# Performance work log

Measured on AMD Instinct MI355X. Metric: run time of the kernel, lower is better.

The kernel has to match this reference:

```python
import jax, jax.numpy as jnp
import numpy as np

B, NS, NT, C = 32, 1000, 100, 256
LAMBDA_GIOU, LAMBDA_L1 = 10.0, 1.0


def _lsa(cost):
    """Hungarian / Jonker-Volgenant shortest-augmenting-path (numpy, O(n^2 m)).
    Matches scipy.optimize.linear_sum_assignment for rectangular matrices."""
    cost = np.asarray(cost, dtype=np.float64)
    transposed = cost.shape[0] > cost.shape[1]
    if transposed:
        cost = cost.T
    n, m = cost.shape  # n <= m
    INF = np.inf
    u = np.zeros(n + 1)
    v = np.zeros(m + 1)
    p = np.zeros(m + 1, dtype=np.int64)   # p[j] = row (1-based) assigned to col j
    way = np.zeros(m + 1, dtype=np.int64)
    for i in range(1, n + 1):
        p[0] = i
        j0 = 0
        minv = np.full(m + 1, INF)
        used = np.zeros(m + 1, dtype=bool)
        while True:
            used[j0] = True
            i0 = p[j0]
            cur = cost[i0 - 1, :] - u[i0] - v[1:]
            free = ~used[1:]
            better = free & (cur < minv[1:])
            minv[1:][better] = cur[better]
            way[1:][better] = j0
            masked = np.where(free, minv[1:], INF)
            j1 = int(np.argmin(masked)) + 1
            delta = masked[j1 - 1]
            u[p[used]] += delta
            v[used] -= delta
            minv[~used] -= delta
            j0 = j1
            if p[j0] == 0:
                break
        while j0:
            j1 = way[j0]
            p[j0] = p[j1]
            j0 = j1
    rows = p[1:] - 1
    cols = np.arange(m)
    keep = rows >= 0
    rows, cols = rows[keep], cols[keep]
    if transposed:
        rows, cols = cols, rows
    order = np.argsort(rows)
    return rows[order], cols[order]


def _pairwise_cost(logits, classes, sb, tb):
    """Per-batch (Ns,Nt) cost = CE(logits_s, class_t) + 10*(1-GIoU(box_s, box_t)) + L1mean."""
    Bc, Ns, Cd = logits.shape
    Nt = classes.shape[1]
    # Cross entropy: logsumexp over classes minus logit at target class (identical
    # math to the torch expand+flatten CE, without the Ns*Nt*C copy).
    lse = jax.nn.logsumexp(logits, axis=-1)  # (B,Ns)
    picked = jnp.take_along_axis(
        logits, jnp.broadcast_to(classes[:, None, :], (Bc, Ns, Nt)), axis=2)  # (B,Ns,Nt)
    ce = lse[:, :, None] - picked
    # Pairwise GIoU (boxes in xyxy)
    s = sb[:, :, None, :]  # (B,Ns,1,4)
    t = tb[:, None, :, :]  # (B,1,Nt,4)
    ix1 = jnp.maximum(s[..., 0], t[..., 0])
    iy1 = jnp.maximum(s[..., 1], t[..., 1])
    ix2 = jnp.minimum(s[..., 2], t[..., 2])
    iy2 = jnp.minimum(s[..., 3], t[..., 3])
    inter = jnp.clip(ix2 - ix1, 0.0) * jnp.clip(iy2 - iy1, 0.0)
    area_s = (s[..., 2] - s[..., 0]) * (s[..., 3] - s[..., 1])
    area_t = (t[..., 2] - t[..., 0]) * (t[..., 3] - t[..., 1])
    union = area_s + area_t - inter
    iou = inter / union
    cx1 = jnp.minimum(s[..., 0], t[..., 0])
    cy1 = jnp.minimum(s[..., 1], t[..., 1])
    cx2 = jnp.maximum(s[..., 2], t[..., 2])
    cy2 = jnp.maximum(s[..., 3], t[..., 3])
    carea = (cx2 - cx1) * (cy2 - cy1)
    giou = iou - (carea - union) / carea
    l1 = jnp.abs(s - t).mean(axis=-1)  # (B,Ns,Nt)
    return ce + LAMBDA_GIOU * (1.0 - giou) + LAMBDA_L1 * l1


def _valid_boxes(key, b, n):
    p = jax.random.uniform(key, (b, n, 2, 2), dtype=jnp.float32)
    lo = p.min(axis=2)
    hi = p.max(axis=2)
    return jnp.concatenate([lo, hi], axis=-1)  # (b,n,4) xyxy, x1<x2, y1<y2


def setup_inputs() -> dict:
    key = jax.random.key(0)
    k1, k2, k3, k4 = jax.random.split(key, 4)
    return {
        "source_class_logits": jax.random.normal(k1, (B, NS, C), dtype=jnp.float32),
        "target_classes": jax.random.randint(k2, (B, NT), 0, C, dtype=jnp.int32),
        "source_boxes": _valid_boxes(k3, B, NS),
        "target_boxes": _valid_boxes(k4, B, NT),
    }


def reference(source_class_logits, target_classes, source_boxes, target_boxes):
    cost = _pairwise_cost(source_class_logits, target_classes, source_boxes, target_boxes)
    cost_np = np.asarray(cost)
    rows_l, cols_l = [], []
    for b in range(cost_np.shape[0]):  # assignment is inherently per-matrix / host-side
        r, c = _lsa(cost_np[b])
        rows_l.append(r)
        cols_l.append(c)
    rows = jnp.asarray(np.stack(rows_l))  # (B, min(Ns,Nt))
    cols = jnp.asarray(np.stack(cols_l))
    bidx = jnp.arange(cost.shape[0])[:, None]
    return cost[bidx, rows, cols].mean(axis=1)  # (B,)
```

## Files before the change

### kernel.cpp

```cpp
#include <hip/hip_runtime.h>
#include <math.h>

#define NSRC 1000
#define NTGT 100
#define NCLS 256
#define NB   32
#define NSP  1024
#define PAD_IDX(j) ((j) + ((j) >> 4))
#define LDSN (NSP + (NSP >> 4))
#define AUCTION_EPS 0.01f

__global__ __launch_bounds__(256) void lse_kernel(const float* __restrict__ logits,
                                                  float* __restrict__ lse) {
    int wid  = threadIdx.x >> 6;
    int lane = threadIdx.x & 63;
    int row0 = blockIdx.x * 32 + wid * 8;
    #pragma unroll 2
    for (int r = 0; r < 8; ++r) {
        int row = row0 + r;
        float4 v4 = reinterpret_cast<const float4*>(logits + (size_t)row * NCLS)[lane];
        float m = fmaxf(fmaxf(v4.x, v4.y), fmaxf(v4.z, v4.w));
        #pragma unroll
        for (int off = 32; off >= 1; off >>= 1) m = fmaxf(m, __shfl_xor(m, off));
        float s = expf(v4.x - m) + expf(v4.y - m) + expf(v4.z - m) + expf(v4.w - m);
        #pragma unroll
        for (int off = 32; off >= 1; off >>= 1) s += __shfl_xor(s, off);
        if (lane == 0) lse[row] = m + logf(s);
    }
}

__global__ __launch_bounds__(256) void cost_kernel(const float* __restrict__ logits,
                                                   const int*   __restrict__ tcls,
                                                   const float* __restrict__ sbox,
                                                   const float* __restrict__ tbox,
                                                   const float* __restrict__ lse,
                                                   float*       __restrict__ cost,
                                                   float*       __restrict__ urow_g,
                                                   int*         __restrict__ jmin_g,
                                                   float*       __restrict__ m2_g) {
    int b  = blockIdx.x & 31;
    int t  = blockIdx.x >> 5;
    int bt = b * NTGT + t;
    int cls = tcls[bt];
    float4 tb = reinterpret_cast<const float4*>(tbox)[bt];
    float area_t = (tb.z - tb.x) * (tb.w - tb.y);
    float* crow = cost + (size_t)bt * NSP;
    float m1 = 1e38f, m2 = 1e38f; int mi = 0x7fffffff;
    for (int s = threadIdx.x; s < NSP; s += 256) {
        if (s >= NSRC) { crow[s] = 1e30f; continue; }
        int gs = b * NSRC + s;
        float4 sb = reinterpret_cast<const float4*>(sbox)[gs];
        float ce = lse[gs] - logits[(size_t)gs * NCLS + cls];
        float ix1 = fmaxf(sb.x, tb.x), iy1 = fmaxf(sb.y, tb.y);
        float ix2 = fminf(sb.z, tb.z), iy2 = fminf(sb.w, tb.w);
        float inter = fmaxf(ix2 - ix1, 0.f) * fmaxf(iy2 - iy1, 0.f);
        float area_s = (sb.z - sb.x) * (sb.w - sb.y);
        float uni = area_s + area_t - inter;
        float iou = inter / uni;
        float cx1 = fminf(sb.x, tb.x), cy1 = fminf(sb.y, tb.y);
        float cx2 = fmaxf(sb.z, tb.z), cy2 = fmaxf(sb.w, tb.w);
        float carea = (cx2 - cx1) * (cy2 - cy1);
        float giou = iou - (carea - uni) / carea;
        float l1 = 0.25f * (fabsf(sb.x - tb.x) + fabsf(sb.y - tb.y) +
                            fabsf(sb.z - tb.z) + fabsf(sb.w - tb.w));
        float c = ce + 10.0f * (1.0f - giou) + l1;
        crow[s] = c;
        if (c < m1) { m2 = m1; m1 = c; mi = s; }
        else if (c < m2) m2 = c;
    }
    #pragma unroll
    for (int off = 32; off >= 1; off >>= 1) {
        float om1 = __shfl_xor(m1, off);
        float om2 = __shfl_xor(m2, off);
        int   oi  = __shfl_xor(mi, off);
        bool take = (om1 < m1) || (om1 == m1 && oi < mi);
        float lose = take ? m1 : om1;
        m1 = take ? om1 : m1;
        mi = take ? oi  : mi;
        m2 = fminf(fminf(m2, om2), lose);
    }
    __shared__ float smin[4], smin2[4];
    __shared__ int   sidx[4];
    int wid = threadIdx.x >> 6, lane = threadIdx.x & 63;
    if (lane == 0) { smin[wid] = m1; smin2[wid] = m2; sidx[wid] = mi; }
    __syncthreads();
    if (threadIdx.x == 0) {
        #pragma unroll
        for (int w = 1; w < 4; ++w) {
            float om1 = smin[w], om2 = smin2[w]; int oi = sidx[w];
            bool take = (om1 < m1) || (om1 == m1 && oi < mi);
            float lose = take ? m1 : om1;
            m1 = take ? om1 : m1;
            mi = take ? oi  : mi;
            m2 = fminf(fminf(m2, om2), lose);
        }
        urow_g[bt] = m1;
        jmin_g[bt] = mi;
        m2_g[bt]   = m2;
    }
}

__global__ __launch_bounds__(64) void lsa_kernel(const float* __restrict__ cost,
                                                 const float* __restrict__ urow_g,
                                                 const int*   __restrict__ jmin_g,
                                                 const float* __restrict__ m2_g,
                                                 float* __restrict__ out) {
    int b    = blockIdx.x;
    int lane = threadIdx.x;
    const float* C = cost + (size_t)b * NTGT * NSP;
    __shared__ int   way[LDSN];
    __shared__ int   pcol[LDSN];
    __shared__ float uu[LDSN];
    __shared__ float vsh[LDSN];
    __shared__ float urow[NTGT];
    __shared__ float m2s[NTGT];
    __shared__ int   jmin[NTGT];
    __shared__ int   done[NTGT];
    __shared__ int   queue[768];
    for (int t = lane; t < LDSN; t += 64) {
        pcol[t] = -1; uu[t] = 0.f; vsh[t] = 0.f; way[t] = 0x7fffffff;
    }
    for (int t = lane; t < NTGT; t += 64) {
        urow[t] = urow_g[b * NTGT + t];
        jmin[t] = jmin_g[b * NTGT + t];
        m2s[t]  = m2_g[b * NTGT + t];
    }
    float v[16], d[16];
    #pragma unroll
    for (int k = 0; k < 16; ++k) v[k] = 0.f;
    int base = lane * 16;
    __syncthreads();

    for (int r = lane; r < NTGT; r += 64) atomicMin(&way[PAD_IDX(jmin[r])], r);
    __syncthreads();
    for (int r = lane; r < NTGT; r += 64) {
        int j = jmin[r];
        int w = (way[PAD_IDX(j)] == r) ? 1 : 0;
        done[r] = w;
        if (w) { pcol[PAD_IDX(j)] = r; uu[PAD_IDX(j)] = urow[r]; }
    }
    __syncthreads();

    int qt = 0;
    #pragma unroll
    for (int r0 = 0; r0 < 128; r0 += 64) {
        int r = r0 + lane;
        bool act = (r < NTGT) && !done[r];
        unsigned long long mask = __ballot(act);
        if (act) queue[qt + __popcll(mask & ((1ull << lane) - 1ull))] = r;
        qt += __popcll(mask);
    }
    int qinit = qt;
    __syncthreads();

    int qh = 0, steps = 0;
    while (qh < qt && steps < 600) {
        ++steps;
        int  i      = queue[qh];
        bool isInit = (qh < qinit);
        ++qh;
        int j1; float m1, m2;
        int   pj  = jmin[i];
        float vpj = vsh[PAD_IDX(pj)];
        if (isInit && vpj == 0.0f) {
            j1 = pj; m1 = urow[i]; m2 = m2s[i];
        } else {
            const float4* row4 = reinterpret_cast<const float4*>(C + (size_t)i * NSP + base);
            m1 = 1e38f; m2 = 1e38f; j1 = 0x7fffffff;
            #pragma unroll
            for (int q = 0; q < 4; ++q) {
                float4 c4 = row4[q];
                float vals[4] = {c4.x - v[4*q+0], c4.y - v[4*q+1],
                                 c4.z - v[4*q+2], c4.w - v[4*q+3]};
                #pragma unroll
                for (int e = 0; e < 4; ++e) {
                    float val = vals[e];
                    if (val < m1) { m2 = m1; m1 = val; j1 = base + 4*q + e; }
                    else m2 = fminf(m2, val);
                }
            }
            #pragma unroll
            for (int off = 32; off >= 1; off >>= 1) {
                float om1 = __shfl_xor(m1, off);
                float om2 = __shfl_xor(m2, off);
                int   oj1 = __shfl_xor(j1, off);
                bool take = (om1 < m1) || (om1 == m1 && oj1 < j1);
                float lose = take ? m1 : om1;
                m1 = take ? om1 : m1;
                j1 = take ? oj1 : j1;
                m2 = fminf(fminf(m2, om2), lose);
            }
        }
        float delta = fmaxf(m2 - m1, AUCTION_EPS);
        int old = pcol[PAD_IDX(j1)];
        if ((j1 >> 4) == lane) {
            #pragma unroll
            for (int k = 0; k < 16; ++k)
                if ((j1 & 15) == k) { v[k] -= delta; vsh[PAD_IDX(j1)] = v[k]; }
        }
        if (lane == 0) {
            pcol[PAD_IDX(j1)] = i;
            uu[PAD_IDX(j1)]   = m1 + delta;
            urow[i] = m1 + delta;
            done[i] = 1;
            if (old >= 0) { queue[qt] = old; done[old] = 0; }
        }
        if (old >= 0) qt++;
        __syncthreads();
    }
    __syncthreads();

    for (int i = 0; i < NTGT; ++i) {
        if (done[i]) continue;
        float ui = urow[i];
        {
            const float4* row4 = reinterpret_cast<const float4*>(C + (size_t)i * NSP + base);
            #pragma unroll
            for (int q = 0; q < 4; ++q) {
                float4 c4 = row4[q];
                d[4*q+0] = c4.x - ui - v[4*q+0];
                d[4*q+1] = c4.y - ui - v[4*q+1];
                d[4*q+2] = c4.z - ui - v[4*q+2];
                d[4*q+3] = c4.w - ui - v[4*q+3];
            }
        }
        #pragma unroll
        for (int k = 0; k < 16; ++k) way[PAD_IDX(base + k)] = -1;
        unsigned int used = 0;
        float Df = 0.f;
        int jf = -1;

        for (int it = 0; it < NTGT + 3; ++it) {
            float lmin = 1e38f;
            #pragma unroll
            for (int k = 0; k < 16; ++k) {
                float val = ((used >> k) & 1u) ? 1e38f : d[k];
                lmin = fminf(lmin, val);
            }
            float wmin = lmin;
            #pragma unroll
            for (int off = 32; off >= 1; off >>= 1) wmin = fminf(wmin, __shfl_xor(wmin, off));
            unsigned long long msk = __ballot(lmin == wmin);
            int src = __ffsll(msk) - 1;
            int myk = -1;
            #pragma unroll
            for (int k = 15; k >= 0; --k)
                if (!((used >> k) & 1u) && d[k] == wmin) myk = k;
            int j0 = __shfl(base + myk, src);
            if (j0 < 0) break;
            int pj0 = pcol[PAD_IDX(j0)];
            if (pj0 < 0) { Df = wmin; jf = j0; break; }
            if ((j0 >> 4) == lane) used |= 1u << (j0 & 15);
            float uref = uu[PAD_IDX(j0)];
            float sft  = wmin - uref;
            const float4* rr = reinterpret_cast<const float4*>(C + (size_t)pj0 * NSP + base);
            float cr[16];
            #pragma unroll
            for (int q = 0; q < 4; ++q) {
                float4 c4 = rr[q];
                cr[4*q+0] = c4.x; cr[4*q+1] = c4.y; cr[4*q+2] = c4.z; cr[4*q+3] = c4.w;
            }
            #pragma unroll
            for (int k = 0; k < 16; ++k) {
                float cand = sft + cr[k] - v[k];
                bool upd = (cand < d[k]) && !((used >> k) & 1u);
                if (upd) { d[k] = cand; way[PAD_IDX(base + k)] = j0; }
            }
        }

        if (jf >= 0) {
            #pragma unroll
            for (int k = 0; k < 16; ++k) {
                if ((used >> k) & 1u) {
                    float diff = Df - d[k];
                    v[k] -= diff;
                    uu[PAD_IDX(base + k)] += diff;
                }
            }
        }
        __syncthreads();
        if (lane == 0 && jf >= 0) {
            int j = jf;
            for (int g = 0; g < NSP; ++g) {
                int jp = way[PAD_IDX(j)];
                if (jp < 0) { pcol[PAD_IDX(j)] = i; uu[PAD_IDX(j)] = ui + Df; break; }
                pcol[PAD_IDX(j)] = pcol[PAD_IDX(jp)];
                uu[PAD_IDX(j)]   = uu[PAD_IDX(jp)];
                j = jp;
            }
            done[i] = 1;
        }
        __syncthreads();
    }

    float acc = 0.f;
    #pragma unroll
    for (int k = 0; k < 16; ++k) {
        int j = base + k;
        if (j < NSRC) {
            int r = pcol[PAD_IDX(j)];
            if (r >= 0) acc += C[(size_t)r * NSP + j];
        }
    }
    #pragma unroll
    for (int off = 32; off >= 1; off >>= 1) acc += __shfl_xor(acc, off);
    if (lane == 0) out[b] = acc * (1.0f / NTGT);
}

extern "C" void kernel_launch(void* const* d_in, const int* in_sizes, int n_in,
                              void* d_out, int out_size, void* d_ws, size_t ws_size,
                              hipStream_t stream) {
    const float* logits = (const float*)d_in[0];
    const int*   tcls   = (const int*)  d_in[1];
    const float* sbox   = (const float*)d_in[2];
    const float* tbox   = (const float*)d_in[3];
    float* out = (float*)d_out;

    float* lse    = (float*)d_ws;
    float* cost   = lse + 32768;
    float* urow_g = cost + (size_t)NB * NTGT * NSP;
    int*   jmin_g = (int*)(urow_g + NB * NTGT);
    float* m2_g   = (float*)(jmin_g + NB * NTGT);

    lse_kernel <<<1000,      256, 0, stream>>>(logits, lse);
    cost_kernel<<<NB * NTGT, 256, 0, stream>>>(logits, tcls, sbox, tbox, lse, cost,
                                               urow_g, jmin_g, m2_g);
    lsa_kernel <<<NB,        64,  0, stream>>>(cost, urow_g, jmin_g, m2_g, out);
}
```

Before: 150.7 us.

## Run auction bidding with four concurrent waves per batch in LSA kernel

```diff
diff --git a/kernel.cpp b/kernel.cpp
--- a/kernel.cpp
+++ b/kernel.cpp
@@ -9,6 +9,9 @@
 #define PAD_IDX(j) ((j) + ((j) >> 4))
 #define LDSN (NSP + (NSP >> 4))
 #define AUCTION_EPS 0.01f
+#define NWAVES 4
+#define ROUND_CAP 128
+
 
 __global__ __launch_bounds__(256) void lse_kernel(const float* __restrict__ logits,
                                                   float* __restrict__ lse) {
@@ -100,13 +103,15 @@
     }
 }
 
-__global__ __launch_bounds__(64) void lsa_kernel(const float* __restrict__ cost,
-                                                 const float* __restrict__ urow_g,
-                                                 const int*   __restrict__ jmin_g,
-                                                 const float* __restrict__ m2_g,
-                                                 float* __restrict__ out) {
+__global__ __launch_bounds__(256) void lsa_kernel(const float* __restrict__ cost,
+                                                  const float* __restrict__ urow_g,
+                                                  const int*   __restrict__ jmin_g,
+                                                  const float* __restrict__ m2_g,
+                                                  float* __restrict__ out) {
     int b    = blockIdx.x;
-    int lane = threadIdx.x;
+    int tid  = threadIdx.x;
+    int wv   = tid >> 6;
+    int lane = tid & 63;
     const float* C = cost + (size_t)b * NTGT * NSP;
     __shared__ int   way[LDSN];
     __shared__ int   pcol[LDSN];
@@ -116,24 +121,25 @@
     __shared__ float m2s[NTGT];
     __shared__ int   jmin[NTGT];
     __shared__ int   done[NTGT];
-    __shared__ int   queue[768];
-    for (int t = lane; t < LDSN; t += 64) {
+    __shared__ int   qbuf[1024];
+    __shared__ int   qstate[2];
+    __shared__ int   srow[NWAVES], scol[NWAVES];
+    __shared__ float sm1[NWAVES], sm2[NWAVES], svscan[NWAVES];
+
+    for (int t = tid; t < LDSN; t += 256) {
         pcol[t] = -1; uu[t] = 0.f; vsh[t] = 0.f; way[t] = 0x7fffffff;
     }
-    for (int t = lane; t < NTGT; t += 64) {
+    for (int t = tid; t < NTGT; t += 256) {
         urow[t] = urow_g[b * NTGT + t];
         jmin[t] = jmin_g[b * NTGT + t];
         m2s[t]  = m2_g[b * NTGT + t];
     }
-    float v[16], d[16];
-    #pragma unroll
-    for (int k = 0; k < 16; ++k) v[k] = 0.f;
-    int base = lane * 16;
-    __syncthreads();
-
-    for (int r = lane; r < NTGT; r += 64) atomicMin(&way[PAD_IDX(jmin[r])], r);
-    __syncthreads();
-    for (int r = lane; r < NTGT; r += 64) {
+    if (tid == 0) { qstate[0] = 0; qstate[1] = 0; }
+    __syncthreads();
+
+    for (int r = tid; r < NTGT; r += 256) atomicMin(&way[PAD_IDX(jmin[r])], r);
+    __syncthreads();
+    for (int r = tid; r < NTGT; r += 256) {
         int j = jmin[r];
         int w = (way[PAD_IDX(j)] == r) ? 1 : 0;
         done[r] = w;
@@ -141,79 +147,106 @@
     }
     __syncthreads();
 
-    int qt = 0;
-    #pragma unroll
-    for (int r0 = 0; r0 < 128; r0 += 64) {
-        int r = r0 + lane;
-        bool act = (r < NTGT) && !done[r];
-        unsigned long long mask = __ballot(act);
-        if (act) queue[qt + __popcll(mask & ((1ull << lane) - 1ull))] = r;
-        qt += __popcll(mask);
-    }
-    int qinit = qt;
-    __syncthreads();
-
-    int qh = 0, steps = 0;
-    while (qh < qt && steps < 600) {
-        ++steps;
-        int  i      = queue[qh];
-        bool isInit = (qh < qinit);
-        ++qh;
-        int j1; float m1, m2;
-        int   pj  = jmin[i];
-        float vpj = vsh[PAD_IDX(pj)];
-        if (isInit && vpj == 0.0f) {
-            j1 = pj; m1 = urow[i]; m2 = m2s[i];
-        } else {
-            const float4* row4 = reinterpret_cast<const float4*>(C + (size_t)i * NSP + base);
-            m1 = 1e38f; m2 = 1e38f; j1 = 0x7fffffff;
-            #pragma unroll
-            for (int q = 0; q < 4; ++q) {
-                float4 c4 = row4[q];
-                float vals[4] = {c4.x - v[4*q+0], c4.y - v[4*q+1],
-                                 c4.z - v[4*q+2], c4.w - v[4*q+3]};
-                #pragma unroll
-                for (int e = 0; e < 4; ++e) {
-                    float val = vals[e];
-                    if (val < m1) { m2 = m1; m1 = val; j1 = base + 4*q + e; }
-                    else m2 = fminf(m2, val);
-                }
-            }
-            #pragma unroll
-            for (int off = 32; off >= 1; off >>= 1) {
-                float om1 = __shfl_xor(m1, off);
-                float om2 = __shfl_xor(m2, off);
-                int   oj1 = __shfl_xor(j1, off);
-                bool take = (om1 < m1) || (om1 == m1 && oj1 < j1);
-                float lose = take ? m1 : om1;
-                m1 = take ? om1 : m1;
-                j1 = take ? oj1 : j1;
-                m2 = fminf(fminf(m2, om2), lose);
-            }
-        }
-        float delta = fmaxf(m2 - m1, AUCTION_EPS);
-        int old = pcol[PAD_IDX(j1)];
-        if ((j1 >> 4) == lane) {
-            #pragma unroll
-            for (int k = 0; k < 16; ++k)
-                if ((j1 & 15) == k) { v[k] -= delta; vsh[PAD_IDX(j1)] = v[k]; }
-        }
-        if (lane == 0) {
-            pcol[PAD_IDX(j1)] = i;
-            uu[PAD_IDX(j1)]   = m1 + delta;
-            urow[i] = m1 + delta;
-            done[i] = 1;
-            if (old >= 0) { queue[qt] = old; done[old] = 0; }
-        }
-        if (old >= 0) qt++;
+    if (tid < 64) {
+        int qt = 0;
+        #pragma unroll
+        for (int r0 = 0; r0 < 128; r0 += 64) {
+            int r = r0 + lane;
+            bool act = (r < NTGT) && !done[r];
+            unsigned long long mask = __ballot(act);
+            if (act) qbuf[qt + __popcll(mask & ((1ull << lane) - 1ull))] = r;
+            qt += __popcll(mask);
+        }
+        if (lane == 0) qstate[1] = qt;
+    }
+    __syncthreads();
+
+    int base = lane * 16;
+
+    for (int round = 0; round < ROUND_CAP; ++round) {
+        int qh = qstate[0], qt = qstate[1];
+        int navail = qt - qh;
+        if (navail <= 0) break;
+        int take = navail < NWAVES ? navail : NWAVES;
+        if (wv < take) {
+            int i = qbuf[(qh + wv) & 1023];
+            int j1; float m1, m2;
+            int pj = jmin[i];
+            if (vsh[PAD_IDX(pj)] == 0.0f) {
+                j1 = pj; m1 = urow[i]; m2 = m2s[i];
+            } else {
+                const float4* row4 = reinterpret_cast<const float4*>(C + (size_t)i * NSP + base);
+                m1 = 1e38f; m2 = 1e38f; j1 = 0x7fffffff;
+                #pragma unroll
+                for (int q = 0; q < 4; ++q) {
+                    float4 c4 = row4[q];
+                    float vals[4];
+                    vals[0] = c4.x - vsh[PAD_IDX(base + 4*q + 0)];
+                    vals[1] = c4.y - vsh[PAD_IDX(base + 4*q + 1)];
+                    vals[2] = c4.z - vsh[PAD_IDX(base + 4*q + 2)];
+                    vals[3] = c4.w - vsh[PAD_IDX(base + 4*q + 3)];
+                    #pragma unroll
+                    for (int e = 0; e < 4; ++e) {
+                        float val = vals[e];
+                        if (val < m1) { m2 = m1; m1 = val; j1 = base + 4*q + e; }
+                        else m2 = fminf(m2, val);
+                    }
+                }
+                #pragma unroll
+                for (int off = 32; off >= 1; off >>= 1) {
+                    float om1 = __shfl_xor(m1, off);
+                    float om2 = __shfl_xor(m2, off);
+                    int   oj1 = __shfl_xor(j1, off);
+                    bool take2 = (om1 < m1) || (om1 == m1 && oj1 < j1);
+                    float lose = take2 ? m1 : om1;
+                    m1 = take2 ? om1 : m1;
+                    j1 = take2 ? oj1 : j1;
+                    m2 = fminf(fminf(m2, om2), lose);
+                }
+            }
+            if (lane == 0) {
+                srow[wv] = i; scol[wv] = j1; sm1[wv] = m1; sm2[wv] = m2;
+                svscan[wv] = vsh[PAD_IDX(j1)];
+            }
+        }
         __syncthreads();
+        if (tid == 0) {
+            int qt2 = qstate[1];
+            for (int s = 0; s < take; ++s) {
+                int i = srow[s], j1 = scol[s];
+                int pj1 = PAD_IDX(j1);
+                if (vsh[pj1] == svscan[s]) {
+                    float delta = fmaxf(sm2[s] - sm1[s], AUCTION_EPS);
+                    int old = pcol[pj1];
+                    vsh[pj1]  = svscan[s] - delta;
+                    pcol[pj1] = i;
+                    uu[pj1]   = sm1[s] + delta;
+                    urow[i]   = sm1[s] + delta;
+                    done[i]   = 1;
+                    if (old >= 0) { qbuf[qt2 & 1023] = old; ++qt2; done[old] = 0; }
+                } else {
+                    qbuf[qt2 & 1023] = i; ++qt2;
+                }
+            }
+            qstate[0] = qstate[0] + take;
+            qstate[1] = qt2;
+        }
+        __syncthreads();
+    }
+
+    float v[16], d[16];
+    if (tid < 64) {
+        #pragma unroll
+        for (int k = 0; k < 16; ++k) v[k] = vsh[PAD_IDX(base + k)];
     }
     __syncthreads();
 
     for (int i = 0; i < NTGT; ++i) {
         if (done[i]) continue;
         float ui = urow[i];
-        {
+        float Df = 0.f;
+        int jf = -1;
+        if (tid < 64) {
             const float4* row4 = reinterpret_cast<const float4*>(C + (size_t)i * NSP + base);
             #pragma unroll
             for (int q = 0; q < 4; ++q) {
@@ -223,63 +256,61 @@
                 d[4*q+2] = c4.z - ui - v[4*q+2];
                 d[4*q+3] = c4.w - ui - v[4*q+3];
             }
-        }
-        #pragma unroll
-        for (int k = 0; k < 16; ++k) way[PAD_IDX(base + k)] = -1;
-        unsigned int used = 0;
-        float Df = 0.f;
-        int jf = -1;
-
-        for (int it = 0; it < NTGT + 3; ++it) {
-            float lmin = 1e38f;
             #pragma unroll
-            for (int k = 0; k < 16; ++k) {
-                float val = ((used >> k) & 1u) ? 1e38f : d[k];
-                lmin = fminf(lmin, val);
-            }
-            float wmin = lmin;
-            #pragma unroll
-            for (int off = 32; off >= 1; off >>= 1) wmin = fminf(wmin, __shfl_xor(wmin, off));
-            unsigned long long msk = __ballot(lmin == wmin);
-            int src = __ffsll(msk) - 1;
-            int myk = -1;
-            #pragma unroll
-            for (int k = 15; k >= 0; --k)
-                if (!((used >> k) & 1u) && d[k] == wmin) myk = k;
-            int j0 = __shfl(base + myk, src);
-            if (j0 < 0) break;
-            int pj0 = pcol[PAD_IDX(j0)];
-            if (pj0 < 0) { Df = wmin; jf = j0; break; }
-            if ((j0 >> 4) == lane) used |= 1u << (j0 & 15);
-            float uref = uu[PAD_IDX(j0)];
-            float sft  = wmin - uref;
-            const float4* rr = reinterpret_cast<const float4*>(C + (size_t)pj0 * NSP + base);
-            float cr[16];
-            #pragma unroll
-            for (int q = 0; q < 4; ++q) {
-                float4 c4 = rr[q];
-                cr[4*q+0] = c4.x; cr[4*q+1] = c4.y; cr[4*q+2] = c4.z; cr[4*q+3] = c4.w;
-            }
-            #pragma unroll
-            for (int k = 0; k < 16; ++k) {
-                float cand = sft + cr[k] - v[k];
-                bool upd = (cand < d[k]) && !((used >> k) & 1u);
-                if (upd) { d[k] = cand; way[PAD_IDX(base + k)] = j0; }
-            }
-        }
-
-        if (jf >= 0) {
-            #pragma unroll
-            for (int k = 0; k < 16; ++k) {
-                if ((used >> k) & 1u) {
-                    float diff = Df - d[k];
-                    v[k] -= diff;
-                    uu[PAD_IDX(base + k)] += diff;
+            for (int k = 0; k < 16; ++k) way[PAD_IDX(base + k)] = -1;
+            unsigned int used = 0;
+
+            for (int it = 0; it < NTGT + 3; ++it) {
+                float lmin = 1e38f;
+                #pragma unroll
+                for (int k = 0; k < 16; ++k) {
+                    float val = ((used >> k) & 1u) ? 1e38f : d[k];
+                    lmin = fminf(lmin, val);
+                }
+                float wmin = lmin;
+                #pragma unroll
+                for (int off = 32; off >= 1; off >>= 1) wmin = fminf(wmin, __shfl_xor(wmin, off));
+                unsigned long long msk = __ballot(lmin == wmin);
+                int src = __ffsll(msk) - 1;
+                int myk = -1;
+                #pragma unroll
+                for (int k = 15; k >= 0; --k)
+                    if (!((used >> k) & 1u) && d[k] == wmin) myk = k;
+                int j0 = __shfl(base + myk, src);
+                if (j0 < 0) break;
+                int pj0 = pcol[PAD_IDX(j0)];
+                if (pj0 < 0) { Df = wmin; jf = j0; break; }
+                if ((j0 >> 4) == lane) used |= 1u << (j0 & 15);
+                float uref = uu[PAD_IDX(j0)];
+                float sft  = wmin - uref;
+                const float4* rr = reinterpret_cast<const float4*>(C + (size_t)pj0 * NSP + base);
+                float cr[16];
+                #pragma unroll
+                for (int q = 0; q < 4; ++q) {
+                    float4 c4 = rr[q];
+                    cr[4*q+0] = c4.x; cr[4*q+1] = c4.y; cr[4*q+2] = c4.z; cr[4*q+3] = c4.w;
+                }
+                #pragma unroll
+                for (int k = 0; k < 16; ++k) {
+                    float cand = sft + cr[k] - v[k];
+                    bool upd = (cand < d[k]) && !((used >> k) & 1u);
+                    if (upd) { d[k] = cand; way[PAD_IDX(base + k)] = j0; }
+                }
+            }
+
+            if (jf >= 0) {
+                #pragma unroll
+                for (int k = 0; k < 16; ++k) {
+                    if ((used >> k) & 1u) {
+                        float diff = Df - d[k];
+                        v[k] -= diff;
+                        uu[PAD_IDX(base + k)] += diff;
+                    }
                 }
             }
         }
         __syncthreads();
-        if (lane == 0 && jf >= 0) {
+        if (tid == 0 && jf >= 0) {
             int j = jf;
             for (int g = 0; g < NSP; ++g) {
                 int jp = way[PAD_IDX(j)];
@@ -293,18 +324,20 @@
         __syncthreads();
     }
 
-    float acc = 0.f;
-    #pragma unroll
-    for (int k = 0; k < 16; ++k) {
-        int j = base + k;
-        if (j < NSRC) {
-            int r = pcol[PAD_IDX(j)];
-            if (r >= 0) acc += C[(size_t)r * NSP + j];
-        }
-    }
-    #pragma unroll
-    for (int off = 32; off >= 1; off >>= 1) acc += __shfl_xor(acc, off);
-    if (lane == 0) out[b] = acc * (1.0f / NTGT);
+    if (tid < 64) {
+        float acc = 0.f;
+        #pragma unroll
+        for (int k = 0; k < 16; ++k) {
+            int j = base + k;
+            if (j < NSRC) {
+                int r = pcol[PAD_IDX(j)];
+                if (r >= 0) acc += C[(size_t)r * NSP + j];
+            }
+        }
+        #pragma unroll
+        for (int off = 32; off >= 1; off >>= 1) acc += __shfl_xor(acc, off);
+        if (lane == 0) out[b] = acc * (1.0f / NTGT);
+    }
 }
 
 extern "C" void kernel_launch(void* const* d_in, const int* in_sizes, int n_in,
@@ -325,5 +358,5 @@
     lse_kernel <<<1000,      256, 0, stream>>>(logits, lse);
     cost_kernel<<<NB * NTGT, 256, 0, stream>>>(logits, tcls, sbox, tbox, lse, cost,
                                                urow_g, jmin_g, m2_g);
-    lsa_kernel <<<NB,        64,  0, stream>>>(cost, urow_g, jmin_g, m2_g, out);
+    lsa_kernel <<<NB,        256, 0, stream>>>(cost, urow_g, jmin_g, m2_g, out);
 }
```

Result: faster. 128.6 us (-14.7%).
